# Kernel optimization log

Measured on AMD Instinct MI355X. Metric: run time of the kernel, lower is better.

## Reference

```python
import jax, jax.numpy as jnp
import numpy as np

KH, KW = 3, 3
PAD = 1
C_IN, C_OUT = 64, 128


def unfold(x, kh, kw, pad):
    # x: (B, C, H, W) -> (B, C, kh*kw, H*W), torch.nn.functional.unfold ordering
    B, C, H, W = x.shape
    xp = jnp.pad(x, ((0, 0), (0, 0), (pad, pad), (pad, pad)))
    patches = jnp.stack(
        [xp[:, :, i:i + H, j:j + W] for i in range(kh) for j in range(kw)],
        axis=2,
    )  # (B, C, K, H, W)
    return patches.reshape(B, C, kh * kw, H * W)


def setup_inputs() -> dict:
    key = jax.random.key(0)
    k1, k2, k3 = jax.random.split(key, 3)
    B, H, W = 8, 128, 128
    inp = jax.random.normal(k1, (B, C_IN, H, W), dtype=jnp.float32)
    g_buffer = jax.random.uniform(k2, (B, 2, H, W), dtype=jnp.float32)
    # weights param as in torch: (1, C*kh*kw, 1, out_channels), kaiming-uniform-ish
    wdepth = C_IN * KH * KW
    bound = float(np.sqrt(6.0 / wdepth))
    weights = jax.random.uniform(k3, (1, wdepth, 1, C_OUT), dtype=jnp.float32,
                                 minval=-bound, maxval=bound)
    bias = jnp.zeros((C_OUT,), dtype=jnp.float32)
    return {"input": inp, "g_buffer": g_buffer, "weights": weights, "bias": bias}


def reference(input, g_buffer, weights, bias):
    B, C, H, W = input.shape
    K = KH * KW
    L = H * W
    depth = 2.0 * (g_buffer[:, -1:, :, :] - 0.5)  # (B, 1, H, W)

    input_unf = unfold(input, KH, KW, PAD)          # (B, C, K, L)
    depth_unf = unfold(depth, KH, KW, PAD)          # (B, 1, K, L)

    # bilateral depth weighting
    dfeat = depth_unf - depth.reshape(B, 1, 1, L)   # (B, 1, K, L)
    dfeat = jnp.sum(dfeat * dfeat, axis=1)          # (B, K, L)
    wf = jnp.exp(-dfeat)
    wf = 9.0 * wf / jnp.sum(wf, axis=1, keepdims=True)  # (B, K, L)

    filt = input_unf * wf[:, None, :, :]            # (B, C, K, L)
    filt = filt.reshape(B, C * K, L)

    W2 = weights.reshape(C_OUT, C * K)              # raw reshape, matches torch .view
    out_unf = jnp.einsum('bkl,ok->bol', filt, W2)   # (B, C_OUT, L)
    out = out_unf.reshape(B, C_OUT, H, W) + bias[None, :, None, None]
    return out
```

## Files before the change

### kernel.cpp

```cpp
#include <hip/hip_runtime.h>
#include <hip/hip_bf16.h>
#include <stdint.h>

typedef _Float16 f16x8 __attribute__((ext_vector_type(8)));
typedef float    f32x4 __attribute__((ext_vector_type(4)));

#define CIN   64
#define COUT  128
#define HH    128
#define WW    128
#define BB    8

#define TROW  130
#define ROWBYTES (130 * 128)
#define TSIZE ((size_t)BB * TROW * ROWBYTES)

#define LROWB (34 * 128)
#define NCHKT (4 * 272)

#define AS1 __attribute__((address_space(1)))
#define AS3 __attribute__((address_space(3)))


__global__ void prep_plus(const float* __restrict__ wflat, _Float16* __restrict__ bp,
                          _Float16* __restrict__ T) {
    int gid = blockIdx.x * 256 + threadIdx.x;
    if (gid < 8 * 18 * 64 * 8) {
        int j = gid & 7;
        int l = (gid >> 3) & 63;
        int s = (gid >> 9) % 18;
        int n = gid / (18 * 512);
        int o = n * 16 + (l & 15);
        int c = ((s & 1) << 5) + ((l >> 4) << 3) + j;
        int k = s >> 1;
        bp[gid] = (_Float16)wflat[o * 576 + c * 9 + k];
        return;
    }
    int h = gid - 8 * 18 * 64 * 8;
    if (h < 16 * 1040) {
        int row = h / 1040, c = h - row * 1040;
        int b = row >> 1, yp = (row & 1) * 129;
        f16x8 z = {};
        *(f16x8*)((char*)T + (size_t)(b * TROW + yp) * ROWBYTES + c * 16) = z;
    }
}

__global__ __launch_bounds__(256) void transpose_pass(const float* __restrict__ inp,
                                                      _Float16* __restrict__ T) {
    __shared__ float sT[64][129];
    const int b   = blockIdx.x >> 7;
    const int y   = blockIdx.x & 127;
    const int tid = threadIdx.x;

    const float* ib = inp + ((long)b * CIN * HH + y) * WW;
    const int xq = tid & 31, c8 = tid >> 5;
    #pragma unroll
    for (int i = 0; i < 8; ++i) {
        int c = c8 * 8 + i;
        float4 v = *(const float4*)(ib + (long)c * (HH * WW) + (xq << 2));
        *(float4*)&sT[c][xq << 2] = v;
    }
    __syncthreads();

    const int x  = tid & 127;
    const int ch = tid >> 7;
    char* rowp = (char*)T + (size_t)(b * TROW + y + 1) * ROWBYTES + (size_t)(x + 1) * 128;
    const int sw = (x + 1) & 7;
    for (int c0 = ch * 8; c0 < 64; c0 += 16) {
        f16x8 v;
        #pragma unroll
        for (int j = 0; j < 8; ++j) v[j] = (_Float16)sT[c0 + j][x];
        *(f16x8*)(rowp + (((c0 >> 3) ^ sw) << 4)) = v;
    }
    if (tid < 16) {
        char* basep = (char*)T + (size_t)(b * TROW + y + 1) * ROWBYTES
                    + ((tid >> 3) ? 129 * 128 : 0) + (tid & 7) * 16;
        f16x8 z = {};
        *(f16x8*)basep = z;
    }
}

__global__ __launch_bounds__(256, 4) void depthcnn_main(
    const _Float16* __restrict__ T, const float* __restrict__ gbuf,
    const float* __restrict__ bias, const _Float16* __restrict__ aprep,
    float* __restrict__ out)
{
    __shared__ __align__(1024) char sIn[4 * LROWB];
    __shared__ _Float16 sWf[2][9][36];

    const int blk    = blockIdx.x;
    const int b      = blk & 7;
    const int rest   = blk >> 3;
    const int strip  = rest & 63;
    const int xq     = rest >> 6;
    const int ystart = strip << 1;
    const int x0     = xq << 5;

    const int tid  = threadIdx.x;
    const int wave = tid >> 6;
    const int lane = tid & 63;
    const int oi   = wave;
    const int l15  = lane & 15;
    const int g4   = lane >> 4;

    {
        const char* Tb = (const char*)T + ((size_t)b * TROW + ystart) * ROWBYTES
                       + (size_t)x0 * 128;
        #pragma unroll
        for (int tt = 0; tt < 5; ++tt) {
            int t = tt * 256 + tid;
            if (t < NCHKT) {
                int tr = t / 272, c = t - tr * 272;
                __builtin_amdgcn_global_load_lds(
                    (const AS1 uint32_t*)(Tb + (size_t)tr * ROWBYTES + c * 16),
                    (AS3 uint32_t*)(sIn + tr * LROWB + c * 16), 16, 0, 0);
            }
        }
    }

    if (tid < 64) {
        const int r = tid >> 5, pxl = tid & 31, x = x0 + pxl, y = ystart + r;
        const float* g = gbuf + ((size_t)b * 2 + 1) * (HH * WW);
        float dc = 2.f * (g[y * WW + x] - 0.5f);
        float e[9];
        float ssum = 0.f;
        #pragma unroll
        for (int k = 0; k < 9; ++k) {
            int yy = y + (k / 3) - 1;
            int xx = x + (k % 3) - 1;
            float dn = 0.f;
            if ((unsigned)yy < 128u && (unsigned)xx < 128u)
                dn = 2.f * (g[yy * WW + xx] - 0.5f);
            float df = dn - dc;
            float ek = __expf(-df * df);
            e[k] = ek;
            ssum += ek;
        }
        float sc = 9.f / ssum;
        #pragma unroll
        for (int k = 0; k < 9; ++k) sWf[r][k][pxl] = (_Float16)(e[k] * sc);
    }

    __syncthreads();

    f32x4 acc[2][2][2];
    #pragma unroll
    for (int r = 0; r < 2; ++r)
        #pragma unroll
        for (int t2 = 0; t2 < 2; ++t2)
            #pragma unroll
            for (int pt = 0; pt < 2; ++pt)
                acc[r][t2][pt] = (f32x4){0.f, 0.f, 0.f, 0.f};

    const f16x8* __restrict__ ap = (const f16x8*)aprep;

    f16x8 af[2][2][2];
    #pragma unroll
    for (int t2 = 0; t2 < 2; ++t2)
        #pragma unroll
        for (int ch = 0; ch < 2; ++ch)
            af[0][t2][ch] = ap[(size_t)(((oi * 2 + t2) * 18) + ch) * 64 + lane];

    #pragma unroll
    for (int k = 0; k < 9; ++k) {
        if (k < 8) {
            #pragma unroll
            for (int t2 = 0; t2 < 2; ++t2)
                #pragma unroll
                for (int ch = 0; ch < 2; ++ch)
                    af[(k + 1) & 1][t2][ch] =
                        ap[(size_t)(((oi * 2 + t2) * 18) + 2 * (k + 1) + ch) * 64 + lane];
        }
        const int dy = k / 3;
        const int dx = k - 3 * dy;
        #pragma unroll
        for (int r = 0; r < 2; ++r) {
            _Float16 wh[2];
            #pragma unroll
            for (int pt = 0; pt < 2; ++pt)
                wh[pt] = sWf[r][k][(pt << 4) + l15];
            #pragma unroll
            for (int ch = 0; ch < 2; ++ch) {
                f16x8 bf[2];
                #pragma unroll
                for (int pt = 0; pt < 2; ++pt) {
                    const int xl  = (pt << 4) + l15 + dx;
                    const int off = (r + dy) * LROWB + (xl << 7)
                                  + ((((ch << 2) | g4) ^ (xl & 7)) << 4);
                    f16x8 iv = *(const f16x8*)(sIn + off);
                    f16x8 w8 = {wh[pt], wh[pt], wh[pt], wh[pt],
                                wh[pt], wh[pt], wh[pt], wh[pt]};
                    bf[pt] = iv * w8;
                }
                #pragma unroll
                for (int t2 = 0; t2 < 2; ++t2)
                    #pragma unroll
                    for (int pt = 0; pt < 2; ++pt)
                        acc[r][t2][pt] = __builtin_amdgcn_mfma_f32_16x16x32_f16(
                            af[k & 1][t2][ch], bf[pt], acc[r][t2][pt], 0, 0, 0);
            }
        }
    }

    float* ob = out + (size_t)b * COUT * (HH * WW) + x0;
    #pragma unroll
    for (int r = 0; r < 2; ++r) {
        const int y = ystart + r;
        #pragma unroll
        for (int t2 = 0; t2 < 2; ++t2) {
            #pragma unroll
            for (int pt = 0; pt < 2; ++pt) {
                #pragma unroll
                for (int r4 = 0; r4 < 4; ++r4) {
                    const int o = (oi << 5) + (t2 << 4) + (g4 << 2) + r4;
                    ob[(size_t)o * (HH * WW) + (size_t)y * WW + (pt << 4) + l15]
                        = acc[r][t2][pt][r4] + bias[o];
                }
            }
        }
    }
}

extern "C" void kernel_launch(void* const* d_in, const int* in_sizes, int n_in,
                              void* d_out, int out_size, void* d_ws, size_t ws_size,
                              hipStream_t stream) {
    const float* inp  = (const float*)d_in[0];
    const float* gbuf = (const float*)d_in[1];
    const float* wts  = (const float*)d_in[2];
    const float* bias = (const float*)d_in[3];

    _Float16* T  = (_Float16*)d_ws;
    _Float16* bp = (_Float16*)((char*)d_ws + TSIZE);

    hipLaunchKernelGGL(prep_plus, dim3(353), dim3(256), 0, stream, wts, bp, T);
    hipLaunchKernelGGL(transpose_pass, dim3(BB * HH), dim3(256), 0, stream, inp, T);
    hipLaunchKernelGGL(depthcnn_main, dim3(2048), dim3(256), 0, stream,
                       T, gbuf, bias, bp, (float*)d_out);
}
```

Measured before the change: 50.31 us.

## Stagger kernel-tap order per wave, spread depth weights across waves, hoist weight loads

Each wave now starts its 9-tap loop at a different tap offset, so the four waves hit different LDS rows and weight addresses at the same time. The depth-weight exp computation is spread over lane group 0 of all four waves instead of being done by wave 0 alone. The first weight-fragment loads are issued before that computation. LDS addressing is precomputed per tap, and s_setprio wraps the MFMA bursts. The aim is less LDS bank contention, less load imbalance before the barrier, and more overlap of memory with compute. In exchange, tap indexing is now runtime per wave rather than compile-time.

Result: no change. 50.21 us (-0.2%).

```diff
diff --git a/kernel.cpp b/kernel.cpp
--- a/kernel.cpp
+++ b/kernel.cpp
@@ -102,6 +102,7 @@
     const int oi   = wave;
     const int l15  = lane & 15;
     const int g4   = lane >> 4;
+    const int off  = wave << 1;
 
     {
         const char* Tb = (const char*)T + ((size_t)b * TROW + ystart) * ROWBYTES
@@ -118,8 +119,22 @@
         }
     }
 
-    if (tid < 64) {
-        const int r = tid >> 5, pxl = tid & 31, x = x0 + pxl, y = ystart + r;
+    const f16x8* __restrict__ ap = (const f16x8*)aprep;
+    const char* wp0 = (const char*)ap + (size_t)((oi * 2 + 0) * 18) * 1024 + lane * 16;
+    const char* wp1 = (const char*)ap + (size_t)((oi * 2 + 1) * 18) * 1024 + lane * 16;
+    f16x8 af[2][2][2];
+    {
+        const char* q0 = wp0 + (off << 11);
+        const char* q1 = wp1 + (off << 11);
+        af[0][0][0] = *(const f16x8*)(q0);
+        af[0][0][1] = *(const f16x8*)(q0 + 1024);
+        af[0][1][0] = *(const f16x8*)(q1);
+        af[0][1][1] = *(const f16x8*)(q1 + 1024);
+    }
+
+    if (g4 == 0) {
+        const int item = (wave << 4) | l15;
+        const int r = item >> 5, pxl = item & 31, x = x0 + pxl, y = ystart + r;
         const float* g = gbuf + ((size_t)b * 2 + 1) * (HH * WW);
         float dc = 2.f * (g[y * WW + x] - 0.5f);
         float e[9];
@@ -143,6 +158,8 @@
 
     __syncthreads();
 
+    const char* bwf = (const char*)&sWf[0][0][0] + l15 * 2;
+
     f32x4 acc[2][2][2];
     #pragma unroll
     for (int r = 0; r < 2; ++r)
@@ -152,52 +169,52 @@
             for (int pt = 0; pt < 2; ++pt)
                 acc[r][t2][pt] = (f32x4){0.f, 0.f, 0.f, 0.f};
 
-    const f16x8* __restrict__ ap = (const f16x8*)aprep;
-
-    f16x8 af[2][2][2];
-    #pragma unroll
-    for (int t2 = 0; t2 < 2; ++t2)
-        #pragma unroll
-        for (int ch = 0; ch < 2; ++ch)
-            af[0][t2][ch] = ap[(size_t)(((oi * 2 + t2) * 18) + ch) * 64 + lane];
-
-    #pragma unroll
-    for (int k = 0; k < 9; ++k) {
-        if (k < 8) {
-            #pragma unroll
-            for (int t2 = 0; t2 < 2; ++t2)
-                #pragma unroll
-                for (int ch = 0; ch < 2; ++ch)
-                    af[(k + 1) & 1][t2][ch] =
-                        ap[(size_t)(((oi * 2 + t2) * 18) + 2 * (k + 1) + ch) * 64 + lane];
-        }
-        const int dy = k / 3;
-        const int dx = k - 3 * dy;
+    #pragma unroll
+    for (int i = 0; i < 9; ++i) {
+        int k = i + off; k = (k >= 9) ? k - 9 : k;
+        if (i < 8) {
+            int kn = k + 1; kn = (kn >= 9) ? kn - 9 : kn;
+            const char* q0 = wp0 + (kn << 11);
+            const char* q1 = wp1 + (kn << 11);
+            af[(i + 1) & 1][0][0] = *(const f16x8*)(q0);
+            af[(i + 1) & 1][0][1] = *(const f16x8*)(q0 + 1024);
+            af[(i + 1) & 1][1][0] = *(const f16x8*)(q1);
+            af[(i + 1) & 1][1][1] = *(const f16x8*)(q1 + 1024);
+        }
+        const int dy  = (k * 11) >> 5;
+        const int dx  = k - dy * 3;
+        const int xl  = l15 + dx;
+        const int s7  = xl & 7;
+        const int dyb = dy * LROWB;
+        const int kwf = k * 72;
+        const char* cb0 = sIn + ((xl << 7) + ((g4 ^ s7) << 4));
+        const char* cb1 = sIn + ((xl << 7) + (((4 | g4) ^ s7) << 4));
         #pragma unroll
         for (int r = 0; r < 2; ++r) {
             _Float16 wh[2];
             #pragma unroll
             for (int pt = 0; pt < 2; ++pt)
-                wh[pt] = sWf[r][k][(pt << 4) + l15];
+                wh[pt] = *(const _Float16*)(bwf + kwf + (r * 648 + pt * 32));
+            const int rb = dyb + r * LROWB;
             #pragma unroll
             for (int ch = 0; ch < 2; ++ch) {
+                const char* cb = ch ? cb1 : cb0;
                 f16x8 bf[2];
                 #pragma unroll
                 for (int pt = 0; pt < 2; ++pt) {
-                    const int xl  = (pt << 4) + l15 + dx;
-                    const int off = (r + dy) * LROWB + (xl << 7)
-                                  + ((((ch << 2) | g4) ^ (xl & 7)) << 4);
-                    f16x8 iv = *(const f16x8*)(sIn + off);
+                    f16x8 iv = *(const f16x8*)(cb + rb + (pt << 11));
                     f16x8 w8 = {wh[pt], wh[pt], wh[pt], wh[pt],
                                 wh[pt], wh[pt], wh[pt], wh[pt]};
                     bf[pt] = iv * w8;
                 }
+                __builtin_amdgcn_s_setprio(1);
                 #pragma unroll
                 for (int t2 = 0; t2 < 2; ++t2)
                     #pragma unroll
                     for (int pt = 0; pt < 2; ++pt)
                         acc[r][t2][pt] = __builtin_amdgcn_mfma_f32_16x16x32_f16(
-                            af[k & 1][t2][ch], bf[pt], acc[r][t2][pt], 0, 0, 0);
+                            af[i & 1][t2][ch], bf[pt], acc[r][t2][pt], 0, 0, 0);
+                __builtin_amdgcn_s_setprio(0);
             }
         }
     }
```
